# Performance work log

Measured on AMD Instinct MI355X. Metric: run time of the kernel, lower is better.

Reference implementation:

```python
import jax, jax.numpy as jnp
import numpy as np

BLOCK = 32  # GGML Q8_0-style block size: one scale per 32 quantized values


def setup_inputs() -> dict:
    key = jax.random.key(0)
    k1, k2, k3, k4 = jax.random.split(key, 4)
    B, S, IN, OUT = 2, 4096, 4096, 4096
    inp = jax.random.normal(k1, (B, S, IN), dtype=jnp.float32)
    # stored GGUF layout: [in_features, out_features]; torch forward transposes it
    qweight = jax.random.randint(k2, (IN, OUT), -127, 128, dtype=jnp.int32)  # int8 codes
    scales = jax.random.normal(k3, (IN, OUT // BLOCK), dtype=jnp.float32) * 0.01  # per-block scale
    bias = jax.random.normal(k4, (OUT,), dtype=jnp.float32) * 0.02
    return {"input": inp, "qweight": qweight, "scales": scales, "bias": bias}


def _dequantize(qweight, scales, dtype):
    # blockwise dequant: w[i, b*32 + j] = q[i, b*32 + j] * scale[i, b]
    IN, OUT = qweight.shape
    q = qweight.reshape(IN, OUT // BLOCK, BLOCK).astype(dtype)
    return (q * scales[:, :, None].astype(dtype)).reshape(IN, OUT)


def reference(input, qweight, scales, bias):
    # torch: F.linear(x, W_stored.T, b) == x @ W_stored + b with W_stored [IN, OUT]
    w = _dequantize(qweight, scales, input.dtype)  # [IN, OUT]
    return jnp.einsum('bsi,io->bso', input, w) + bias
```

## Files before the change

kernel.cpp:

```cpp
#include <hip/hip_runtime.h>
#include <hip/hip_bf16.h>
#include <stdint.h>


#define M_DIM 8192
#define N_DIM 4096
#define K_DIM 4096
#define NBLK  128

typedef __attribute__((ext_vector_type(8))) short short8;
typedef __attribute__((ext_vector_type(4))) float f32x4;

typedef const __attribute__((address_space(1))) unsigned char* gas;
typedef __attribute__((address_space(3))) unsigned char* las;

__device__ __forceinline__ unsigned pk_bf16(float a, float b) {
  unsigned ua = __builtin_bit_cast(unsigned, a);
  unsigned ub = __builtin_bit_cast(unsigned, b);
  ua += 0x7fffu + ((ua >> 16) & 1u);
  ub += 0x7fffu + ((ub >> 16) & 1u);
  return (ua >> 16) | (ub & 0xffff0000u);
}

__global__ __launch_bounds__(256)
void a_to_bf16(const float* __restrict__ A, ushort* __restrict__ Abf) {
  const long idx = ((long)blockIdx.x * 256 + threadIdx.x) * 8;
  const float4 v0 = *(const float4*)(A + idx);
  const float4 v1 = *(const float4*)(A + idx + 4);
  uint4 p;
  p.x = pk_bf16(v0.x, v0.y);
  p.y = pk_bf16(v0.z, v0.w);
  p.z = pk_bf16(v1.x, v1.y);
  p.w = pk_bf16(v1.z, v1.w);
  *(uint4*)(Abf + idx) = p;
}

__global__ __launch_bounds__(256)
void dequant_transpose(const int* __restrict__ Q, const float* __restrict__ S,
                       ushort* __restrict__ Wt) {
  __shared__ ushort T[64 * 68];
  const int k0 = blockIdx.y * 64;
  const int n0 = blockIdx.x * 64;
  const int t = threadIdx.x;
  const int nl = t & 63;
  const int kb = t >> 6;

  const float sscale = S[0] * 0.0f;
  (void)sscale;

  #pragma unroll
  for (int i = 0; i < 16; ++i) {
    const int kl = kb + i * 4;
    const int k = k0 + kl;
    const int q = Q[(long)k * N_DIM + n0 + nl];
    const float s = S[k * NBLK + ((n0 + nl) >> 5)];
    const float w = (float)q * s;
    unsigned u = __builtin_bit_cast(unsigned, w);
    u += 0x7fffu + ((u >> 16) & 1u);
    T[nl * 68 + kl] = (ushort)(u >> 16);
  }
  __syncthreads();

  const int n = t >> 2;
  const int kc = (t & 3) * 16;
  const ushort* src = &T[n * 68 + kc];
  uint2 a = *(const uint2*)(src + 0);
  uint2 b = *(const uint2*)(src + 4);
  uint2 c = *(const uint2*)(src + 8);
  uint2 d = *(const uint2*)(src + 12);
  uint4 o0 = {a.x, a.y, b.x, b.y};
  uint4 o1 = {c.x, c.y, d.x, d.y};
  ushort* dst = Wt + (long)(n0 + n) * K_DIM + k0 + kc;
  *(uint4*)(dst + 0) = o0;
  *(uint4*)(dst + 8) = o1;
}

__global__ __launch_bounds__(256)
void gemm_bf16(const ushort* __restrict__ Abf, const ushort* __restrict__ Wt,
               const float* __restrict__ bias, float* __restrict__ C) {
  __shared__ __align__(16) ushort Alds[128 * 32];
  __shared__ __align__(16) ushort Blds[128 * 32];

  const int tid = threadIdx.x;
  const int m0 = blockIdx.y * 128;
  const int n0 = blockIdx.x * 128;
  const int wave = tid >> 6;
  const int lane = tid & 63;
  const int wm = (wave >> 1) * 64;
  const int wn = (wave & 1) * 64;
  const int lrow = lane & 15;
  const int quad = lane >> 4;

  const int srow = wave * 16 + (lane >> 2);
  const int skoff = (lane & 3) * 8;

  const ushort* Ag0 = Abf + (long)(m0 + srow) * K_DIM + skoff;
  const ushort* Ag1 = Ag0 + (long)64 * K_DIM;
  const ushort* Bg0 = Wt + (long)(n0 + srow) * K_DIM + skoff;
  const ushort* Bg1 = Bg0 + (long)64 * K_DIM;

  ushort* Al0 = &Alds[wave * 512];
  ushort* Al1 = &Alds[wave * 512 + 2048];
  ushort* Bl0 = &Blds[wave * 512];
  ushort* Bl1 = &Blds[wave * 512 + 2048];

  f32x4 acc[4][4];
  #pragma unroll
  for (int i = 0; i < 4; ++i)
    #pragma unroll
    for (int j = 0; j < 4; ++j)
      acc[i][j] = (f32x4){0.f, 0.f, 0.f, 0.f};

  for (int k0 = 0; k0 < K_DIM; k0 += 32) {
    __builtin_amdgcn_global_load_lds((gas)(Ag0 + k0), (las)Al0, 16, 0, 0);
    __builtin_amdgcn_global_load_lds((gas)(Ag1 + k0), (las)Al1, 16, 0, 0);
    __builtin_amdgcn_global_load_lds((gas)(Bg0 + k0), (las)Bl0, 16, 0, 0);
    __builtin_amdgcn_global_load_lds((gas)(Bg1 + k0), (las)Bl1, 16, 0, 0);
    __syncthreads();

    short8 afrag[4], bfrag[4];
    #pragma unroll
    for (int t = 0; t < 4; ++t) {
      afrag[t] = *(const short8*)&Alds[(wm + t * 16 + lrow) * 32 + quad * 8];
      bfrag[t] = *(const short8*)&Blds[(wn + t * 16 + lrow) * 32 + quad * 8];
    }
    #pragma unroll
    for (int mt = 0; mt < 4; ++mt)
      #pragma unroll
      for (int nt = 0; nt < 4; ++nt)
        acc[mt][nt] = __builtin_amdgcn_mfma_f32_16x16x32_bf16(afrag[mt], bfrag[nt],
                                                              acc[mt][nt], 0, 0, 0);
    __syncthreads();
  }

  #pragma unroll
  for (int nt = 0; nt < 4; ++nt) {
    const int n = n0 + wn + nt * 16 + lrow;
    const float bv = bias[n];
    #pragma unroll
    for (int mt = 0; mt < 4; ++mt) {
      const int mbase = m0 + wm + mt * 16 + quad * 4;
      #pragma unroll
      for (int r = 0; r < 4; ++r) {
        C[(long)(mbase + r) * N_DIM + n] = acc[mt][nt][r] + bv;
      }
    }
  }
}

__global__ __launch_bounds__(256)
void gguf_gemm_fused(const float* __restrict__ A, const int* __restrict__ Q,
                     const float* __restrict__ S, const float* __restrict__ bias,
                     float* __restrict__ C) {
  __shared__ __align__(16) ushort Alds[128 * 32];
  __shared__ __align__(16) ushort Blds[128 * 32];
  const int tid = threadIdx.x;
  const int m0 = blockIdx.y * 128;
  const int n0 = blockIdx.x * 128;
  const int wave = tid >> 6, lane = tid & 63;
  const int wm = (wave >> 1) * 64, wn = (wave & 1) * 64;
  const int lrow = lane & 15, quad = lane >> 4;
  const int ar = tid >> 2, ac = (tid & 3) * 4;
  const int c8a = ((ar >> 1) & 3) << 3;
  const int bn = tid & 127, bkc = (tid >> 7) * 16;
  const int c8b = ((bn >> 1) & 3) << 3;
  const float* Abase = A + (long)(m0 + ar) * K_DIM + ac;
  const int* Qbase = Q + (long)bkc * N_DIM + n0 + bn;
  const float* Sbase = S + (long)bkc * NBLK + ((n0 + bn) >> 5);
  f32x4 acc[4][4];
  #pragma unroll
  for (int i = 0; i < 4; ++i)
    #pragma unroll
    for (int j = 0; j < 4; ++j) acc[i][j] = (f32x4){0.f, 0.f, 0.f, 0.f};
  for (int k0 = 0; k0 < K_DIM; k0 += 32) {
    #pragma unroll
    for (int i = 0; i < 2; ++i)
      #pragma unroll
      for (int j = 0; j < 2; ++j) {
        const float4 v = *(const float4*)(Abase + (long)i * 64 * K_DIM + k0 + j * 16);
        uint2 p; p.x = pk_bf16(v.x, v.y); p.y = pk_bf16(v.z, v.w);
        const int k = ac + j * 16;
        *(uint2*)&Alds[(ar + i * 64) * 32 + (k ^ c8a)] = p;
      }
    {
      const int* qp = Qbase + (long)k0 * N_DIM;
      const float* sp = Sbase + (long)k0 * NBLK;
      unsigned w[8];
      #pragma unroll
      for (int i = 0; i < 8; ++i) {
        const int q0 = qp[(2 * i) * N_DIM];
        const int q1 = qp[(2 * i + 1) * N_DIM];
        const float s0 = sp[(2 * i) * NBLK];
        const float s1 = sp[(2 * i + 1) * NBLK];
        w[i] = pk_bf16((float)q0 * s0, (float)q1 * s1);
      }
      uint4 g0 = {w[0], w[1], w[2], w[3]};
      uint4 g1 = {w[4], w[5], w[6], w[7]};
      *(uint4*)&Blds[bn * 32 + (bkc ^ c8b)] = g0;
      *(uint4*)&Blds[bn * 32 + ((bkc + 8) ^ c8b)] = g1;
    }
    __syncthreads();
    short8 afrag[4], bfrag[4];
    #pragma unroll
    for (int t = 0; t < 4; ++t) {
      const int mrow = wm + t * 16 + lrow;
      afrag[t] = *(const short8*)&Alds[mrow * 32 + ((quad * 8) ^ (((mrow >> 1) & 3) << 3))];
      const int nrow = wn + t * 16 + lrow;
      bfrag[t] = *(const short8*)&Blds[nrow * 32 + ((quad * 8) ^ (((nrow >> 1) & 3) << 3))];
    }
    #pragma unroll
    for (int mt = 0; mt < 4; ++mt)
      #pragma unroll
      for (int nt = 0; nt < 4; ++nt)
        acc[mt][nt] = __builtin_amdgcn_mfma_f32_16x16x32_bf16(afrag[mt], bfrag[nt],
                                                              acc[mt][nt], 0, 0, 0);
    __syncthreads();
  }
  #pragma unroll
  for (int nt = 0; nt < 4; ++nt) {
    const int n = n0 + wn + nt * 16 + lrow;
    const float bv = bias[n];
    #pragma unroll
    for (int mt = 0; mt < 4; ++mt) {
      const int mbase = m0 + wm + mt * 16 + quad * 4;
      #pragma unroll
      for (int r = 0; r < 4; ++r)
        C[(long)(mbase + r) * N_DIM + n] = acc[mt][nt][r] + bv;
    }
  }
}

extern "C" void kernel_launch(void* const* d_in, const int* in_sizes, int n_in,
                              void* d_out, int out_size, void* d_ws, size_t ws_size,
                              hipStream_t stream) {
  const float* A    = (const float*)d_in[0];
  const int*   Q    = (const int*)d_in[1];
  const float* S    = (const float*)d_in[2];
  const float* bias = (const float*)d_in[3];
  float* C = (float*)d_out;

  const size_t abf_bytes = (size_t)M_DIM * K_DIM * 2;
  const size_t wt_bytes  = (size_t)N_DIM * K_DIM * 2;

  if (ws_size >= abf_bytes + wt_bytes) {
    ushort* Abf = (ushort*)d_ws;
    ushort* Wt  = (ushort*)((char*)d_ws + abf_bytes);
    a_to_bf16<<<(M_DIM * (long)K_DIM) / (256 * 8), 256, 0, stream>>>(A, Abf);
    dim3 gt(N_DIM / 64, K_DIM / 64);
    dequant_transpose<<<gt, 256, 0, stream>>>(Q, S, Wt);
    dim3 grid(N_DIM / 128, M_DIM / 128);
    gemm_bf16<<<grid, 256, 0, stream>>>(Abf, Wt, bias, C);
  } else {
    dim3 grid(N_DIM / 128, M_DIM / 128);
    gguf_gemm_fused<<<grid, 256, 0, stream>>>(A, Q, S, bias, C);
  }
}
```

Baseline: 570.7 us.

## Replace 128x128 bf16 GEMM with 256x256 tile, 4-stage LDS pipeline

Replaces the single-buffered 128x128 GEMM with a 512-thread kernel computing 256x256 output tiles. It streams A and B into a 4-stage LDS ring using async global_load_lds and vmcnt-based waits, so only one barrier sits between compute steps. LDS chunks are XOR-swizzled to avoid bank conflicts, MFMA sections run at raised wave priority, and the block index is remapped for L2 locality. Each wave now holds 128 accumulator floats and the block uses 128KB of LDS, which limits occupancy and adds register pressure.

New measurement: 513.3 us. 1.11x faster.

```diff
diff --git a/kernel.cpp b/kernel.cpp
--- a/kernel.cpp
+++ b/kernel.cpp
@@ -1,5 +1,4 @@
 #include <hip/hip_runtime.h>
-#include <hip/hip_bf16.h>
 #include <stdint.h>
 
 
@@ -7,6 +6,7 @@
 #define N_DIM 4096
 #define K_DIM 4096
 #define NBLK  128
+#define NT    128
 
 typedef __attribute__((ext_vector_type(8))) short short8;
 typedef __attribute__((ext_vector_type(4))) float f32x4;
@@ -44,9 +44,6 @@
   const int t = threadIdx.x;
   const int nl = t & 63;
   const int kb = t >> 6;
-
-  const float sscale = S[0] * 0.0f;
-  (void)sscale;
 
   #pragma unroll
   for (int i = 0; i < 16; ++i) {
@@ -75,75 +72,108 @@
   *(uint4*)(dst + 8) = o1;
 }
 
-__global__ __launch_bounds__(256)
-void gemm_bf16(const ushort* __restrict__ Abf, const ushort* __restrict__ Wt,
-               const float* __restrict__ bias, float* __restrict__ C) {
-  __shared__ __align__(16) ushort Alds[128 * 32];
-  __shared__ __align__(16) ushort Blds[128 * 32];
+__global__ __launch_bounds__(512, 2)
+void gemm256(const ushort* __restrict__ Abf, const ushort* __restrict__ Wt,
+             const float* __restrict__ bias, float* __restrict__ C) {
+  __shared__ __align__(16) ushort lds[4 * 16384];
 
   const int tid = threadIdx.x;
-  const int m0 = blockIdx.y * 128;
-  const int n0 = blockIdx.x * 128;
-  const int wave = tid >> 6;
-  const int lane = tid & 63;
-  const int wm = (wave >> 1) * 64;
-  const int wn = (wave & 1) * 64;
-  const int lrow = lane & 15;
-  const int quad = lane >> 4;
-
-  const int srow = wave * 16 + (lane >> 2);
-  const int skoff = (lane & 3) * 8;
-
-  const ushort* Ag0 = Abf + (long)(m0 + srow) * K_DIM + skoff;
-  const ushort* Ag1 = Ag0 + (long)64 * K_DIM;
-  const ushort* Bg0 = Wt + (long)(n0 + srow) * K_DIM + skoff;
-  const ushort* Bg1 = Bg0 + (long)64 * K_DIM;
-
-  ushort* Al0 = &Alds[wave * 512];
-  ushort* Al1 = &Alds[wave * 512 + 2048];
-  ushort* Bl0 = &Blds[wave * 512];
-  ushort* Bl1 = &Blds[wave * 512 + 2048];
-
-  f32x4 acc[4][4];
-  #pragma unroll
-  for (int i = 0; i < 4; ++i)
+  const int wave = tid >> 6, lane = tid & 63;
+  const int lrow = lane & 15, quad = lane >> 4;
+
+  int id = (int)blockIdx.x;
+  id = (id & 7) * 64 + (id >> 3);
+  const int m0 = (id >> 4) * 256;
+  const int n0 = (id & 15) * 256;
+
+  const int wm = (wave >> 2) * 128;
+  const int wn = (wave & 3) * 64;
+  const int rchunk = (quad ^ ((lrow >> 1) & 3)) * 8;
+
+  const int srow = lane >> 2;
+  const int schunk = ((lane & 3) ^ ((lane >> 3) & 3)) * 8;
+  const ushort* Ag0 = Abf + (long)(m0 + wave * 16 + srow) * K_DIM + schunk;
+  const ushort* Ag1 = Ag0 + (long)128 * K_DIM;
+  const ushort* Bg0 = Wt  + (long)(n0 + wave * 16 + srow) * K_DIM + schunk;
+  const ushort* Bg1 = Bg0 + (long)128 * K_DIM;
+
+  f32x4 acc[8][4];
+  #pragma unroll
+  for (int i = 0; i < 8; ++i)
     #pragma unroll
     for (int j = 0; j < 4; ++j)
       acc[i][j] = (f32x4){0.f, 0.f, 0.f, 0.f};
 
-  for (int k0 = 0; k0 < K_DIM; k0 += 32) {
-    __builtin_amdgcn_global_load_lds((gas)(Ag0 + k0), (las)Al0, 16, 0, 0);
-    __builtin_amdgcn_global_load_lds((gas)(Ag1 + k0), (las)Al1, 16, 0, 0);
-    __builtin_amdgcn_global_load_lds((gas)(Bg0 + k0), (las)Bl0, 16, 0, 0);
-    __builtin_amdgcn_global_load_lds((gas)(Bg1 + k0), (las)Bl1, 16, 0, 0);
-    __syncthreads();
-
-    short8 afrag[4], bfrag[4];
-    #pragma unroll
-    for (int t = 0; t < 4; ++t) {
-      afrag[t] = *(const short8*)&Alds[(wm + t * 16 + lrow) * 32 + quad * 8];
-      bfrag[t] = *(const short8*)&Blds[(wn + t * 16 + lrow) * 32 + quad * 8];
-    }
-    #pragma unroll
-    for (int mt = 0; mt < 4; ++mt)
-      #pragma unroll
-      for (int nt = 0; nt < 4; ++nt)
-        acc[mt][nt] = __builtin_amdgcn_mfma_f32_16x16x32_bf16(afrag[mt], bfrag[nt],
-                                                              acc[mt][nt], 0, 0, 0);
-    __syncthreads();
-  }
-
-  #pragma unroll
-  for (int nt = 0; nt < 4; ++nt) {
-    const int n = n0 + wn + nt * 16 + lrow;
+#define STAGE(kt, ss) do {                                                   \
+    const long ko_ = (long)(kt) * 32;                                        \
+    ushort* As_ = (ushort*)&lds[(ss) * 16384];                               \
+    __builtin_amdgcn_global_load_lds((gas)(Ag0 + ko_),                       \
+        (las)(As_ + wave * 512), 16, 0, 0);                                  \
+    __builtin_amdgcn_global_load_lds((gas)(Ag1 + ko_),                       \
+        (las)(As_ + 4096 + wave * 512), 16, 0, 0);                           \
+    __builtin_amdgcn_global_load_lds((gas)(Bg0 + ko_),                       \
+        (las)(As_ + 8192 + wave * 512), 16, 0, 0);                           \
+    __builtin_amdgcn_global_load_lds((gas)(Bg1 + ko_),                       \
+        (las)(As_ + 12288 + wave * 512), 16, 0, 0);                          \
+  } while (0)
+
+#define COMPUTE(s_) do {                                                     \
+    const ushort* As_ = (const ushort*)&lds[(s_) * 16384];                   \
+    const ushort* Bs_ = As_ + 8192;                                          \
+    short8 af[8], bf[4];                                                     \
+    _Pragma("unroll")                                                        \
+    for (int mt = 0; mt < 8; ++mt)                                           \
+      af[mt] = *(const short8*)&As_[(wm + mt * 16 + lrow) * 32 + rchunk];    \
+    _Pragma("unroll")                                                        \
+    for (int nt2 = 0; nt2 < 4; ++nt2)                                        \
+      bf[nt2] = *(const short8*)&Bs_[(wn + nt2 * 16 + lrow) * 32 + rchunk];  \
+    __builtin_amdgcn_s_setprio(1);                                           \
+    _Pragma("unroll")                                                        \
+    for (int mt = 0; mt < 8; ++mt)                                           \
+      _Pragma("unroll")                                                      \
+      for (int nt2 = 0; nt2 < 4; ++nt2)                                      \
+        acc[mt][nt2] = __builtin_amdgcn_mfma_f32_16x16x32_bf16(              \
+            af[mt], bf[nt2], acc[mt][nt2], 0, 0, 0);                         \
+    __builtin_amdgcn_s_setprio(0);                                           \
+  } while (0)
+
+#define SYNC(n_) do {                                                        \
+    asm volatile("s_waitcnt vmcnt(" #n_ ")" ::: "memory");                   \
+    __builtin_amdgcn_s_barrier();                                            \
+    __builtin_amdgcn_sched_barrier(0);                                       \
+  } while (0)
+
+  STAGE(0, 0);
+  STAGE(1, 1);
+  STAGE(2, 2);
+  SYNC(8);
+
+  #pragma unroll 1
+  for (int t = 0; t < NT - 4; t += 4) {
+    STAGE(t + 3, 3); COMPUTE(0); SYNC(8);
+    STAGE(t + 4, 0); COMPUTE(1); SYNC(8);
+    STAGE(t + 5, 1); COMPUTE(2); SYNC(8);
+    STAGE(t + 6, 2); COMPUTE(3); SYNC(8);
+  }
+  STAGE(127, 3); COMPUTE(0); SYNC(8);
+  COMPUTE(1); SYNC(4);
+  COMPUTE(2); SYNC(0);
+  COMPUTE(3);
+
+#undef STAGE
+#undef COMPUTE
+#undef SYNC
+
+  #pragma unroll
+  for (int nt2 = 0; nt2 < 4; ++nt2) {
+    const int n = n0 + wn + nt2 * 16 + lrow;
     const float bv = bias[n];
     #pragma unroll
-    for (int mt = 0; mt < 4; ++mt) {
+    for (int mt = 0; mt < 8; ++mt) {
       const int mbase = m0 + wm + mt * 16 + quad * 4;
       #pragma unroll
-      for (int r = 0; r < 4; ++r) {
-        C[(long)(mbase + r) * N_DIM + n] = acc[mt][nt][r] + bv;
-      }
+      for (int r = 0; r < 4; ++r)
+        C[(long)(mbase + r) * N_DIM + n] = acc[mt][nt2][r] + bv;
     }
   }
 }
@@ -248,8 +278,7 @@
     a_to_bf16<<<(M_DIM * (long)K_DIM) / (256 * 8), 256, 0, stream>>>(A, Abf);
     dim3 gt(N_DIM / 64, K_DIM / 64);
     dequant_transpose<<<gt, 256, 0, stream>>>(Q, S, Wt);
-    dim3 grid(N_DIM / 128, M_DIM / 128);
-    gemm_bf16<<<grid, 256, 0, stream>>>(Abf, Wt, bias, C);
+    gemm256<<<dim3((M_DIM / 256) * (N_DIM / 256)), dim3(512), 0, stream>>>(Abf, Wt, bias, C);
   } else {
     dim3 grid(N_DIM / 128, M_DIM / 128);
     gguf_gemm_fused<<<grid, 256, 0, stream>>>(A, Q, S, bias, C);
```
